# Kernel tuning notes

Hardware: AMD Instinct MI355X
Metric: run time of the kernel (lower is better)

## Reference

```python
import jax, jax.numpy as jnp
import numpy as np

ND, NA, E, EL, H, F = 100000, 50000, 500000, 200000, 128, 128


def setup_inputs() -> dict:
    key = jax.random.key(0)
    ks = jax.random.split(key, 20)
    def W(k, shape):
        return jax.random.normal(k, shape, dtype=jnp.float32) * 0.05
    inp = {
        'doc_x': jax.random.normal(ks[0], (ND, F), dtype=jnp.float32),
        'author_node_id': jnp.arange(NA, dtype=jnp.int64 if jax.config.jax_enable_x64 else jnp.int32),
        'edge_index': jnp.stack([
            jax.random.randint(ks[1], (E,), 0, ND),   # doc src
            jax.random.randint(ks[2], (E,), 0, NA),   # author dst
        ]),
        'edge_label_index': jnp.stack([
            jax.random.randint(ks[3], (EL,), 0, ND),
            jax.random.randint(ks[4], (EL,), 0, NA),
        ]),
        'doc_lin_W': W(ks[5], (F, H)), 'doc_lin_b': W(ks[6], (H,)),
        'author_emb': W(ks[7], (NA, H)),
        'c1_da_Wl': W(ks[8], (H, H)), 'c1_da_bl': W(ks[9], (H,)), 'c1_da_Wr': W(ks[10], (H, H)),
        'c1_ad_Wl': W(ks[11], (H, H)), 'c1_ad_bl': W(ks[12], (H,)), 'c1_ad_Wr': W(ks[13], (H, H)),
        'c2_da_Wl': W(ks[14], (H, H)), 'c2_da_bl': W(ks[15], (H,)), 'c2_da_Wr': W(ks[16], (H, H)),
        'c2_ad_Wl': W(ks[17], (H, H)), 'c2_ad_bl': W(ks[18], (H,)), 'c2_ad_Wr': W(ks[19], (H, H)),
    }
    return inp


def sage(x_src, x_dst, src, dst, num_dst, Wl, bl, Wr):
    # PyG SAGEConv (aggr='mean'): lin_l(mean_j x_src[j]) + lin_r(x_dst)
    msg = x_src[src]                                            # [E, H]
    agg = jax.ops.segment_sum(msg, dst, num_segments=num_dst)   # [num_dst, H]
    deg = jax.ops.segment_sum(jnp.ones_like(dst, dtype=x_src.dtype), dst, num_segments=num_dst)
    agg = agg / jnp.maximum(deg, 1.0)[:, None]
    return agg @ Wl + bl + x_dst @ Wr


def reference(doc_x, author_node_id, edge_index, edge_label_index,
              doc_lin_W, doc_lin_b, author_emb,
              c1_da_Wl, c1_da_bl, c1_da_Wr, c1_ad_Wl, c1_ad_bl, c1_ad_Wr,
              c2_da_Wl, c2_da_bl, c2_da_Wr, c2_ad_Wl, c2_ad_bl, c2_ad_Wr):
    x_doc = doc_x @ doc_lin_W + doc_lin_b          # [ND, H]
    x_author = author_emb[author_node_id]          # [NA, H]
    src_d, dst_a = edge_index[0], edge_index[1]
    # layer 1 (per-edge-type convs, to_hetero semantics) + ReLU
    h_a = sage(x_doc, x_author, src_d, dst_a, NA, c1_da_Wl, c1_da_bl, c1_da_Wr)
    h_d = sage(x_author, x_doc, dst_a, src_d, ND, c1_ad_Wl, c1_ad_bl, c1_ad_Wr)
    h_a, h_d = jax.nn.relu(h_a), jax.nn.relu(h_d)
    # layer 2
    o_a = sage(h_d, h_a, src_d, dst_a, NA, c2_da_Wl, c2_da_bl, c2_da_Wr)
    o_d = sage(h_a, h_d, dst_a, src_d, ND, c2_ad_Wl, c2_ad_bl, c2_ad_Wr)
    # edge scorer: dot product of gathered endpoint embeddings
    pred = (o_d[edge_label_index[0]] * o_a[edge_label_index[1]]).sum(-1)  # [EL]
    return pred
```

## Files before the change

### kernel.cpp

```cpp
#include <hip/hip_runtime.h>

typedef unsigned short u16;
typedef __attribute__((ext_vector_type(8))) short vbf16x8;
typedef __attribute__((ext_vector_type(4))) float vf32x4;

__device__ __forceinline__ float bf2f(u16 u) {
    union { unsigned int i; float f; } v; v.i = ((unsigned int)u) << 16; return v.f;
}
__device__ __forceinline__ u16 f2bf(float f) {
    union { float f; unsigned int i; } v; v.f = f;
    return (u16)((v.i + 0x7fffu + ((v.i >> 16) & 1u)) >> 16);
}

struct TPack { const float* src[9]; u16* dst[9]; };

#define NBUK 256
#define NBLK_BIN 256
#define SCAP 24
#define OVFCAP 32768
#define PACK_SH 17

__global__ __launch_bounds__(256) void mega_prep_bin(
    TPack p, const float* __restrict__ emb, const int* __restrict__ ids,
    u16* __restrict__ xauth, int NA,
    const int* __restrict__ src, const int* __restrict__ dst,
    unsigned* __restrict__ stageD, unsigned* __restrict__ stageA,
    int* __restrict__ cntD, int* __restrict__ cntA,
    uint2* __restrict__ ovfD, uint2* __restrict__ ovfA, int* __restrict__ ovfn,
    int E, int shD, int shA, int prepB) {
    int b = blockIdx.x;
    if (b >= prepB) {
        __shared__ int lcnt[NBUK];
        int bb = b - prepB;
        const bool isD = bb < NBLK_BIN;
        const int blk = isD ? bb : bb - NBLK_BIN;
        const int* key = isD ? src : dst;
        const int* val = isD ? dst : src;
        const int shift = isD ? shD : shA;
        unsigned* stage = isD ? stageD : stageA;
        int* cnt = isD ? cntD : cntA;
        uint2* ovf = isD ? ovfD : ovfA;
        int* on = ovfn + (isD ? 0 : 1);
        const int per = (E + NBLK_BIN - 1) / NBLK_BIN;
        const int beg = blk * per;
        const int end = min(beg + per, E);
        for (int i = threadIdx.x; i < NBUK; i += 256) lcnt[i] = 0;
        __syncthreads();
        for (int e = beg + (int)threadIdx.x; e < end; e += 256) {
            int k = key[e], v = val[e];
            int bkt = k >> shift;
            int slot = atomicAdd(&lcnt[bkt], 1);
            if (slot < SCAP) {
                unsigned local = (unsigned)(k - (bkt << shift));
                stage[((size_t)bkt * NBLK_BIN + blk) * SCAP + slot] =
                    (local << PACK_SH) | (unsigned)v;
            } else {
                int oi = atomicAdd(on, 1);
                if (oi < OVFCAP) ovf[oi] = make_uint2((unsigned)k, (unsigned)v);
            }
        }
        __syncthreads();
        for (int i = threadIdx.x; i < NBUK; i += 256)
            cnt[(size_t)i * NBLK_BIN + blk] = min(lcnt[i], SCAP);
        return;
    }
    if (b < 576) {
        int mat = b / 64;
        const float* s = p.src[mat];
        u16* d = p.dst[mat];
        int i = (b % 64) * 256 + threadIdx.x;
        int k = i >> 7, n = i & 127;
        d[(size_t)n * 128 + k] = f2bf(s[(size_t)k * 128 + n]);
    } else {
        int gid = (b - 576) * 256 + threadIdx.x;
        if (gid >= NA * 16) return;
        int n = gid >> 4, f = gid & 15;
        int id = ids[n];
        const float* s = emb + (size_t)id * 128 + f * 8;
        float4 lo = *(const float4*)(s);
        float4 hi = *(const float4*)(s + 4);
        u16 o[8] = {f2bf(lo.x), f2bf(lo.y), f2bf(lo.z), f2bf(lo.w),
                    f2bf(hi.x), f2bf(hi.y), f2bf(hi.z), f2bf(hi.w)};
        *(uint4*)(xauth + (size_t)n * 128 + f * 8) = *(const uint4*)o;
    }
}

__global__ __launch_bounds__(256) void bucket_count(
    const unsigned* __restrict__ stageD, const unsigned* __restrict__ stageA,
    const int* __restrict__ cntD, const int* __restrict__ cntA,
    const uint2* __restrict__ ovfD, const uint2* __restrict__ ovfA,
    const int* __restrict__ ovfn,
    int* __restrict__ cnt_d, int* __restrict__ cnt_a,
    int ND, int NA, int shD, int shA) {
    __shared__ int hist[1024];
    __shared__ int segc[NBLK_BIN];
    const bool isD = (int)blockIdx.x < NBUK;
    const int b = isD ? (int)blockIdx.x : (int)blockIdx.x - NBUK;
    const int sh = isD ? shD : shA;
    const int N = isD ? ND : NA;
    const int base = b << sh;
    const int range = min(1 << sh, N - base);
    if (range <= 0) return;
    const unsigned* stage = (isD ? stageD : stageA) + (size_t)b * NBLK_BIN * SCAP;
    const int* scnt = (isD ? cntD : cntA) + (size_t)b * NBLK_BIN;
    const uint2* ovf = isD ? ovfD : ovfA;
    const int nov = min(ovfn[isD ? 0 : 1], OVFCAP);
    int* out = isD ? cnt_d : cnt_a;
    const int tid = threadIdx.x;
    for (int i = tid; i < (1 << sh); i += 256) hist[i] = 0;
    segc[tid] = scnt[tid];
    __syncthreads();
    for (int j = tid; j < NBLK_BIN * SCAP; j += 256) {
        int seg = j / SCAP, slot = j - seg * SCAP;
        if (slot < segc[seg])
            atomicAdd(&hist[stage[j] >> PACK_SH], 1);
    }
    for (int i = tid; i < nov; i += 256) {
        int k = (int)ovf[i].x;
        if ((k >> sh) == b) atomicAdd(&hist[k - base], 1);
    }
    __syncthreads();
    for (int i = tid; i < range; i += 256) out[base + i] = hist[i];
}

__global__ __launch_bounds__(256) void scan1b(
    const int* __restrict__ cnt, int* __restrict__ incl,
    int* __restrict__ bs, int ND, int NA, int NBD) {
    __shared__ int sh[256];
    int b = blockIdx.x, tid = threadIdx.x;
    const int* in; int* out; int N; int lb;
    if (b < NBD) { in = cnt;      out = incl;      N = ND; lb = b; }
    else         { in = cnt + ND; out = incl + ND; N = NA; lb = b - NBD; }
    int gid = lb * 256 + tid;
    int v = gid < N ? in[gid] : 0;
    sh[tid] = v; __syncthreads();
    for (int off = 1; off < 256; off <<= 1) {
        int t = tid >= off ? sh[tid - off] : 0; __syncthreads();
        sh[tid] += t; __syncthreads();
    }
    if (gid < N) out[gid] = sh[tid];
    if (tid == 255) bs[b] = sh[255];
}

__global__ __launch_bounds__(256) void scan2b(int* __restrict__ bs, int NBD, int NBA) {
    __shared__ int sh[256];
    __shared__ int carry;
    int tid = threadIdx.x;
    for (int seg = 0; seg < 2; ++seg) {
        int* p = seg ? bs + NBD : bs;
        int nb = seg ? NBA : NBD;
        if (tid == 0) carry = 0;
        __syncthreads();
        for (int base = 0; base < nb; base += 256) {
            int i = base + tid;
            int v = i < nb ? p[i] : 0;
            sh[tid] = v; __syncthreads();
            for (int off = 1; off < 256; off <<= 1) {
                int t = tid >= off ? sh[tid - off] : 0; __syncthreads();
                sh[tid] += t; __syncthreads();
            }
            if (i < nb) p[i] = carry + sh[tid] - v;
            __syncthreads();
            if (tid == 255) carry += sh[255];
            __syncthreads();
        }
    }
}

__global__ __launch_bounds__(256) void scan3b(
    const int* __restrict__ incl, const int* __restrict__ bs,
    int* __restrict__ offs_d, int* __restrict__ offs_a,
    int ND, int NA, int NBD) {
    int b = blockIdx.x, tid = threadIdx.x;
    if (b < NBD) {
        int gid = b * 256 + tid;
        if (gid < ND) offs_d[gid + 1] = incl[gid] + bs[b];
        if (gid == 0) offs_d[0] = 0;
    } else {
        int gid = (b - NBD) * 256 + tid;
        if (gid < NA) offs_a[gid + 1] = incl[ND + gid] + bs[b];
        if (gid == 0) offs_a[0] = 0;
    }
}

__global__ __launch_bounds__(256) void bucket_fill2(
    const unsigned* __restrict__ stageD, const unsigned* __restrict__ stageA,
    const int* __restrict__ cntD, const int* __restrict__ cntA,
    const uint2* __restrict__ ovfD, const uint2* __restrict__ ovfA,
    const int* __restrict__ ovfn,
    const int* __restrict__ offs_d, const int* __restrict__ offs_a,
    int* __restrict__ nbr_d, int* __restrict__ nbr_a,
    int ND, int NA, int shD, int shA) {
    __shared__ int lcur[1024];
    __shared__ int segc[NBLK_BIN];
    const bool isD = (int)blockIdx.x < NBUK;
    const int b = isD ? (int)blockIdx.x : (int)blockIdx.x - NBUK;
    const int sh = isD ? shD : shA;
    const int N = isD ? ND : NA;
    const int base = b << sh;
    const int range = min(1 << sh, N - base);
    if (range <= 0) return;
    const unsigned* stage = (isD ? stageD : stageA) + (size_t)b * NBLK_BIN * SCAP;
    const int* scnt = (isD ? cntD : cntA) + (size_t)b * NBLK_BIN;
    const uint2* ovf = isD ? ovfD : ovfA;
    const int nov = min(ovfn[isD ? 0 : 1], OVFCAP);
    const int* offs = isD ? offs_d : offs_a;
    int* nbr = isD ? nbr_d : nbr_a;
    const int tid = threadIdx.x;
    for (int i = tid; i < range; i += 256) lcur[i] = offs[base + i];
    segc[tid] = scnt[tid];
    __syncthreads();
    for (int j = tid; j < NBLK_BIN * SCAP; j += 256) {
        int seg = j / SCAP, slot = j - seg * SCAP;
        if (slot < segc[seg]) {
            unsigned pk = stage[j];
            int local = pk >> PACK_SH;
            int v = (int)(pk & ((1u << PACK_SH) - 1u));
            nbr[atomicAdd(&lcur[local], 1)] = v;
        }
    }
    for (int i = tid; i < nov; i += 256) {
        int k = (int)ovf[i].x;
        if ((k >> sh) == b)
            nbr[atomicAdd(&lcur[k - base], 1)] = (int)ovf[i].y;
    }
}

__global__ __launch_bounds__(256) void agg_mean2(
    const u16* __restrict__ xa, const int* __restrict__ offs_a,
    const int* __restrict__ nbr_a, u16* __restrict__ outa, int NA,
    const u16* __restrict__ xd, const int* __restrict__ offs_d,
    const int* __restrict__ nbr_d, u16* __restrict__ outd, int ND) {
    int gid = blockIdx.x * 256 + threadIdx.x;
    int node = gid >> 4, f = gid & 15;
    int lane = threadIdx.x & 63;
    int gbase = lane & 48;
    const u16* x; const int* offs; const int* nbr; u16* out;
    if (node < NA) { x = xa; offs = offs_a; nbr = nbr_a; out = outa; }
    else {
        node -= NA;
        if (node >= ND) return;
        x = xd; offs = offs_d; nbr = nbr_d; out = outd;
    }
    int beg = offs[node], end = offs[node + 1];
    float acc[8] = {0, 0, 0, 0, 0, 0, 0, 0};

    for (int i = beg; i < end; i += 16) {
        int cnt = end - i; if (cnt > 16) cnt = 16;
        int myn = (i + f < end) ? nbr[i + f] : 0;
        int t = 0;
        for (; t + 3 < cnt; t += 4) {
            int i0 = __shfl(myn, gbase + t);
            int i1 = __shfl(myn, gbase + t + 1);
            int i2 = __shfl(myn, gbase + t + 2);
            int i3 = __shfl(myn, gbase + t + 3);
            uint4 q0 = *(const uint4*)(x + (size_t)i0 * 128 + f * 8);
            uint4 q1 = *(const uint4*)(x + (size_t)i1 * 128 + f * 8);
            uint4 q2 = *(const uint4*)(x + (size_t)i2 * 128 + f * 8);
            uint4 q3 = *(const uint4*)(x + (size_t)i3 * 128 + f * 8);
            acc[0] += bf2f((u16)(q0.x & 0xffff)) + bf2f((u16)(q1.x & 0xffff))
                    + bf2f((u16)(q2.x & 0xffff)) + bf2f((u16)(q3.x & 0xffff));
            acc[1] += bf2f((u16)(q0.x >> 16))    + bf2f((u16)(q1.x >> 16))
                    + bf2f((u16)(q2.x >> 16))    + bf2f((u16)(q3.x >> 16));
            acc[2] += bf2f((u16)(q0.y & 0xffff)) + bf2f((u16)(q1.y & 0xffff))
                    + bf2f((u16)(q2.y & 0xffff)) + bf2f((u16)(q3.y & 0xffff));
            acc[3] += bf2f((u16)(q0.y >> 16))    + bf2f((u16)(q1.y >> 16))
                    + bf2f((u16)(q2.y >> 16))    + bf2f((u16)(q3.y >> 16));
            acc[4] += bf2f((u16)(q0.z & 0xffff)) + bf2f((u16)(q1.z & 0xffff))
                    + bf2f((u16)(q2.z & 0xffff)) + bf2f((u16)(q3.z & 0xffff));
            acc[5] += bf2f((u16)(q0.z >> 16))    + bf2f((u16)(q1.z >> 16))
                    + bf2f((u16)(q2.z >> 16))    + bf2f((u16)(q3.z >> 16));
            acc[6] += bf2f((u16)(q0.w & 0xffff)) + bf2f((u16)(q1.w & 0xffff))
                    + bf2f((u16)(q2.w & 0xffff)) + bf2f((u16)(q3.w & 0xffff));
            acc[7] += bf2f((u16)(q0.w >> 16))    + bf2f((u16)(q1.w >> 16))
                    + bf2f((u16)(q2.w >> 16))    + bf2f((u16)(q3.w >> 16));
        }
        for (; t < cnt; ++t) {
            int i0 = __shfl(myn, gbase + t);
            uint4 q0 = *(const uint4*)(x + (size_t)i0 * 128 + f * 8);
            acc[0] += bf2f((u16)(q0.x & 0xffff));
            acc[1] += bf2f((u16)(q0.x >> 16));
            acc[2] += bf2f((u16)(q0.y & 0xffff));
            acc[3] += bf2f((u16)(q0.y >> 16));
            acc[4] += bf2f((u16)(q0.z & 0xffff));
            acc[5] += bf2f((u16)(q0.z >> 16));
            acc[6] += bf2f((u16)(q0.w & 0xffff));
            acc[7] += bf2f((u16)(q0.w >> 16));
        }
    }
    float inv = 1.0f / fmaxf((float)(end - beg), 1.0f);
    u16 o[8];
#pragma unroll
    for (int j = 0; j < 8; ++j) o[j] = f2bf(acc[j] * inv);
    *(uint4*)(out + (size_t)node * 128 + f * 8) = *(const uint4*)o;
}

__global__ __launch_bounds__(256) void doc_gemm4(
    const float* __restrict__ A1f, const u16* __restrict__ W1T,
    const float* __restrict__ bias, u16* __restrict__ out, const int M) {
    __shared__ u16 WS[128 * 128];
    const int tid = threadIdx.x;
    const int lane = tid & 63, wave = tid >> 6;
    const int r15 = lane & 15, kq = lane >> 4;
    const int rowbase = blockIdx.x * 128 + wave * 32;
    const int m0 = rowbase + r15, m1 = rowbase + 16 + r15;
    const bool v0 = rowbase < M, v1 = rowbase + 16 < M;

    const float4 z = {0.f, 0.f, 0.f, 0.f};
    float4 l0[4], h0[4], l1[4], h1[4];
#pragma unroll
    for (int ks = 0; ks < 4; ++ks) {
        const float* p0 = A1f + (size_t)m0 * 128 + ks * 32 + kq * 8;
        const float* p1 = A1f + (size_t)m1 * 128 + ks * 32 + kq * 8;
        l0[ks] = v0 ? *(const float4*)p0 : z;
        h0[ks] = v0 ? *(const float4*)(p0 + 4) : z;
        l1[ks] = v1 ? *(const float4*)p1 : z;
        h1[ks] = v1 ? *(const float4*)(p1 + 4) : z;
    }

#pragma unroll
    for (int i = 0; i < 8; ++i) {
        int L = i * 256 + tid;
        int n = L >> 4, bk = L & 15;
        *(uint4*)(WS + ((size_t)n * 16 + (bk ^ (n & 15))) * 8) =
            *(const uint4*)(W1T + (size_t)L * 8);
    }
    __syncthreads();

    vf32x4 acc0[8], acc1[8];
#pragma unroll
    for (int i = 0; i < 8; ++i) { acc0[i] = (vf32x4)(0.0f); acc1[i] = (vf32x4)(0.0f); }

#pragma unroll
    for (int ks = 0; ks < 4; ++ks) {
        vbf16x8 a0, a1;
        a0[0] = (short)f2bf(l0[ks].x); a0[1] = (short)f2bf(l0[ks].y);
        a0[2] = (short)f2bf(l0[ks].z); a0[3] = (short)f2bf(l0[ks].w);
        a0[4] = (short)f2bf(h0[ks].x); a0[5] = (short)f2bf(h0[ks].y);
        a0[6] = (short)f2bf(h0[ks].z); a0[7] = (short)f2bf(h0[ks].w);
        a1[0] = (short)f2bf(l1[ks].x); a1[1] = (short)f2bf(l1[ks].y);
        a1[2] = (short)f2bf(l1[ks].z); a1[3] = (short)f2bf(l1[ks].w);
        a1[4] = (short)f2bf(h1[ks].x); a1[5] = (short)f2bf(h1[ks].y);
        a1[6] = (short)f2bf(h1[ks].z); a1[7] = (short)f2bf(h1[ks].w);
#pragma unroll
        for (int nt = 0; nt < 8; ++nt) {
            vbf16x8 b = *(const vbf16x8*)(
                WS + ((size_t)(nt * 16 + r15) * 16 + ((ks * 4 + kq) ^ r15)) * 8);
            acc0[nt] = __builtin_amdgcn_mfma_f32_16x16x32_bf16(a0, b, acc0[nt], 0, 0, 0);
            acc1[nt] = __builtin_amdgcn_mfma_f32_16x16x32_bf16(a1, b, acc1[nt], 0, 0, 0);
        }
    }

#pragma unroll
    for (int nt = 0; nt < 8; ++nt) {
        const float bv = bias[nt * 16 + r15];
#pragma unroll
        for (int r = 0; r < 4; ++r) {
            if (v0) out[(size_t)(rowbase + kq * 4 + r) * 128 + nt * 16 + r15] =
                f2bf(acc0[nt][r] + bv);
            if (v1) out[(size_t)(rowbase + 16 + kq * 4 + r) * 128 + nt * 16 + r15] =
                f2bf(acc1[nt][r] + bv);
        }
    }
}

struct SideParams3 {
    const u16* A1b; const u16* W1T;
    const u16* A2b; const u16* W2T;
    const float* bias; u16* out;
    int M; int do_relu; int ntiles; int gblocks;
};
__global__ __launch_bounds__(256) void conv_gemm3(SideParams3 sa, SideParams3 sd) {
    __shared__ u16 WS[2 * 128 * 128];
    const bool isA = (int)blockIdx.x < sa.gblocks;
    SideParams3 P = isA ? sa : sd;
    const int gb = isA ? (int)blockIdx.x : (int)blockIdx.x - sa.gblocks;
    const int tid = threadIdx.x;
    const int lane = tid & 63, wave = tid >> 6;
    const int r15 = lane & 15, kq = lane >> 4;

#pragma unroll
    for (int i = 0; i < 8; ++i) {
        int L = i * 256 + tid;
        int n = L >> 4, bk = L & 15;
        *(uint4*)(WS + ((size_t)n * 16 + (bk ^ (n & 15))) * 8) =
            *(const uint4*)(P.W1T + (size_t)L * 8);
        *(uint4*)(WS + 16384 + ((size_t)n * 16 + (bk ^ (n & 15))) * 8) =
            *(const uint4*)(P.W2T + (size_t)L * 8);
    }
    __syncthreads();
    float bv[8];
#pragma unroll
    for (int nt = 0; nt < 8; ++nt) bv[nt] = P.bias[nt * 16 + r15];

    auto loadA = [&](const u16* Ab, int tile, vbf16x8* fa, vbf16x8* fb) {
        const int rowbase = tile * 128 + wave * 32;
        const int m0 = rowbase + r15, m1 = rowbase + 16 + r15;
        const bool v0 = rowbase < P.M, v1 = rowbase + 16 < P.M;
#pragma unroll
        for (int ks = 0; ks < 4; ++ks) {
            fa[ks] = v0 ? *(const vbf16x8*)(Ab + (size_t)m0 * 128 + ks * 32 + kq * 8)
                        : (vbf16x8)(short)0;
            fb[ks] = v1 ? *(const vbf16x8*)(Ab + (size_t)m1 * 128 + ks * 32 + kq * 8)
                        : (vbf16x8)(short)0;
        }
    };

    vbf16x8 c1a[4], c1b[4], c2a[4], c2b[4], n1a[4], n1b[4];
    if (gb < P.ntiles) loadA(P.A1b, gb, c1a, c1b);
    for (int t = gb; t < P.ntiles; t += P.gblocks) {
        loadA(P.A2b, t, c2a, c2b);
        const int tn = t + P.gblocks;
        if (tn < P.ntiles) loadA(P.A1b, tn, n1a, n1b);

        vf32x4 acc0[8], acc1[8];
#pragma unroll
        for (int i = 0; i < 8; ++i) { acc0[i] = (vf32x4)(0.0f); acc1[i] = (vf32x4)(0.0f); }
#pragma unroll
        for (int ks = 0; ks < 4; ++ks) {
#pragma unroll
            for (int nt = 0; nt < 8; ++nt) {
                vbf16x8 b = *(const vbf16x8*)(
                    WS + ((size_t)(nt * 16 + r15) * 16 + ((ks * 4 + kq) ^ r15)) * 8);
                acc0[nt] = __builtin_amdgcn_mfma_f32_16x16x32_bf16(c1a[ks], b, acc0[nt], 0, 0, 0);
                acc1[nt] = __builtin_amdgcn_mfma_f32_16x16x32_bf16(c1b[ks], b, acc1[nt], 0, 0, 0);
            }
        }
#pragma unroll
        for (int ks = 0; ks < 4; ++ks) {
#pragma unroll
            for (int nt = 0; nt < 8; ++nt) {
                vbf16x8 b = *(const vbf16x8*)(
                    WS + 16384 + ((size_t)(nt * 16 + r15) * 16 + ((ks * 4 + kq) ^ r15)) * 8);
                acc0[nt] = __builtin_amdgcn_mfma_f32_16x16x32_bf16(c2a[ks], b, acc0[nt], 0, 0, 0);
                acc1[nt] = __builtin_amdgcn_mfma_f32_16x16x32_bf16(c2b[ks], b, acc1[nt], 0, 0, 0);
            }
        }

        const int rowbase = t * 128 + wave * 32;
        const bool v0 = rowbase < P.M, v1 = rowbase + 16 < P.M;
#pragma unroll
        for (int nt = 0; nt < 8; ++nt) {
#pragma unroll
            for (int r = 0; r < 4; ++r) {
                if (v0) {
                    float v = acc0[nt][r] + bv[nt];
                    if (P.do_relu) v = fmaxf(v, 0.0f);
                    P.out[(size_t)(rowbase + kq * 4 + r) * 128 + nt * 16 + r15] = f2bf(v);
                }
                if (v1) {
                    float v = acc1[nt][r] + bv[nt];
                    if (P.do_relu) v = fmaxf(v, 0.0f);
                    P.out[(size_t)(rowbase + 16 + kq * 4 + r) * 128 + nt * 16 + r15] = f2bf(v);
                }
            }
        }
#pragma unroll
        for (int ks = 0; ks < 4; ++ks) { c1a[ks] = n1a[ks]; c1b[ks] = n1b[ks]; }
    }
}

__global__ __launch_bounds__(256) void edge_dot(
    const u16* __restrict__ od, const u16* __restrict__ oa,
    const int* __restrict__ i0, const int* __restrict__ i1,
    float* __restrict__ pred, int EL) {
    int gid = blockIdx.x * 256 + threadIdx.x;
    if (gid >= EL * 16) return;
    int e = gid >> 4, f = gid & 15;
    uint4 x = *(const uint4*)(od + (size_t)i0[e] * 128 + f * 8);
    uint4 y = *(const uint4*)(oa + (size_t)i1[e] * 128 + f * 8);
    float s = 0.0f;
    s += bf2f((u16)(x.x & 0xffff)) * bf2f((u16)(y.x & 0xffff));
    s += bf2f((u16)(x.x >> 16))    * bf2f((u16)(y.x >> 16));
    s += bf2f((u16)(x.y & 0xffff)) * bf2f((u16)(y.y & 0xffff));
    s += bf2f((u16)(x.y >> 16))    * bf2f((u16)(y.y >> 16));
    s += bf2f((u16)(x.z & 0xffff)) * bf2f((u16)(y.z & 0xffff));
    s += bf2f((u16)(x.z >> 16))    * bf2f((u16)(y.z >> 16));
    s += bf2f((u16)(x.w & 0xffff)) * bf2f((u16)(y.w & 0xffff));
    s += bf2f((u16)(x.w >> 16))    * bf2f((u16)(y.w >> 16));
    s += __shfl_xor(s, 1);
    s += __shfl_xor(s, 2);
    s += __shfl_xor(s, 4);
    s += __shfl_xor(s, 8);
    if (f == 0) pred[e] = s;
}

extern "C" void kernel_launch(void* const* d_in, const int* in_sizes, int n_in,
                              void* d_out, int out_size, void* d_ws, size_t ws_size,
                              hipStream_t stream) {
    const float* doc_x    = (const float*)d_in[0];
    const int*   auth_id  = (const int*)d_in[1];
    const int*   eidx     = (const int*)d_in[2];
    const int*   elidx    = (const int*)d_in[3];
    const float* W_doc    = (const float*)d_in[4];
    const float* b_doc    = (const float*)d_in[5];
    const float* emb      = (const float*)d_in[6];
    const float* c1_da_Wl = (const float*)d_in[7];
    const float* c1_da_bl = (const float*)d_in[8];
    const float* c1_da_Wr = (const float*)d_in[9];
    const float* c1_ad_Wl = (const float*)d_in[10];
    const float* c1_ad_bl = (const float*)d_in[11];
    const float* c1_ad_Wr = (const float*)d_in[12];
    const float* c2_da_Wl = (const float*)d_in[13];
    const float* c2_da_bl = (const float*)d_in[14];
    const float* c2_da_Wr = (const float*)d_in[15];
    const float* c2_ad_Wl = (const float*)d_in[16];
    const float* c2_ad_bl = (const float*)d_in[17];
    const float* c2_ad_Wr = (const float*)d_in[18];

    const int ND = in_sizes[0] / 128;
    const int NA = in_sizes[1];
    const int E  = in_sizes[2] / 2;
    const int EL = in_sizes[3] / 2;
    const int* e_src = eidx;
    const int* e_dst = eidx + E;
    const int NBD = (ND + 255) / 256, NBA = (NA + 255) / 256;
    const int BA = (NA + 127) / 128, BD = (ND + 127) / 128;
    const int prepB = 576 + (NA * 16 + 255) / 256;

    char* base = (char*)d_ws;
    size_t off = 0;
    auto alloc = [&](size_t bytes) {
        void* p = base + off;
        off = (off + bytes + 255) & ~(size_t)255;
        return p;
    };
    u16*  xdoc  = (u16*)alloc((size_t)ND * 128 * 2);
    u16*  xauth = (u16*)alloc((size_t)NA * 128 * 2);
    u16*  hd    = (u16*)alloc((size_t)ND * 128 * 2);
    u16*  ha    = (u16*)alloc((size_t)NA * 128 * 2);
    u16*  aggA  = (u16*)alloc((size_t)NA * 128 * 2);
    u16*  aggD  = (u16*)alloc((size_t)ND * 128 * 2);
    u16*  wt    = (u16*)alloc((size_t)9 * 128 * 128 * 2);
    int*  cnt   = (int*)alloc((size_t)(ND + NA) * 4);
    int*  incl  = (int*)alloc((size_t)(ND + NA) * 4);
    int*  bs    = (int*)alloc((size_t)(NBD + NBA) * 4);
    int*  offs_d = (int*)alloc((size_t)(ND + 1) * 4);
    int*  offs_a = (int*)alloc((size_t)(NA + 1) * 4);
    int*  nbr_d = (int*)alloc((size_t)E * 4);
    int*  nbr_a = (int*)alloc((size_t)E * 4);
    int*  cntD  = (int*)alloc((size_t)NBUK * NBLK_BIN * 4);
    int*  cntA  = (int*)alloc((size_t)NBUK * NBLK_BIN * 4);
    uint2* ovfD = (uint2*)alloc((size_t)OVFCAP * 8);
    uint2* ovfA = (uint2*)alloc((size_t)OVFCAP * 8);
    int*  ovfn  = (int*)alloc(256);
    (void)ws_size; (void)n_in; (void)out_size;
    u16* od = xdoc;
    u16* oa = xauth;
    unsigned* stageD = (unsigned*)aggD;
    unsigned* stageA = (unsigned*)aggA;

    TPack tp;
    const float* srcs[9] = {W_doc, c1_da_Wl, c1_da_Wr, c1_ad_Wl, c1_ad_Wr,
                            c2_da_Wl, c2_da_Wr, c2_ad_Wl, c2_ad_Wr};
    for (int i = 0; i < 9; ++i) { tp.src[i] = srcs[i]; tp.dst[i] = wt + (size_t)i * 16384; }
    const u16 *WTdoc = wt, *WT_c1daL = wt + 16384, *WT_c1daR = wt + 2 * 16384,
              *WT_c1adL = wt + 3 * 16384, *WT_c1adR = wt + 4 * 16384,
              *WT_c2daL = wt + 5 * 16384, *WT_c2daR = wt + 6 * 16384,
              *WT_c2adL = wt + 7 * 16384, *WT_c2adR = wt + 8 * 16384;

    int shD = 0; while (((ND - 1) >> shD) >= NBUK) ++shD;
    int shA = 0; while (((NA - 1) >> shA) >= NBUK) ++shA;

    hipMemsetAsync(ovfn, 0, 8, stream);
    mega_prep_bin<<<prepB + 2 * NBLK_BIN, 256, 0, stream>>>(
        tp, emb, auth_id, xauth, NA, e_src, e_dst,
        stageD, stageA, cntD, cntA, ovfD, ovfA, ovfn, E, shD, shA, prepB);

    bucket_count<<<2 * NBUK, 256, 0, stream>>>(
        stageD, stageA, cntD, cntA, ovfD, ovfA, ovfn, cnt, cnt + ND,
        ND, NA, shD, shA);

    scan1b<<<NBD + NBA, 256, 0, stream>>>(cnt, incl, bs, ND, NA, NBD);
    scan2b<<<1, 256, 0, stream>>>(bs, NBD, NBA);
    scan3b<<<NBD + NBA, 256, 0, stream>>>(incl, bs, offs_d, offs_a, ND, NA, NBD);

    bucket_fill2<<<2 * NBUK, 256, 0, stream>>>(
        stageD, stageA, cntD, cntA, ovfD, ovfA, ovfn, offs_d, offs_a,
        nbr_d, nbr_a, ND, NA, shD, shA);

    doc_gemm4<<<BD, 256, 0, stream>>>(doc_x, WTdoc, b_doc, xdoc, ND);

    const int aggGrid = ((NA + ND) * 16 + 255) / 256;
    const int gA = (int)(((long)512 * BA) / (BA + BD));
    const int gD = 512 - gA;

    agg_mean2<<<aggGrid, 256, 0, stream>>>(
        xdoc, offs_a, nbr_a, aggA, NA, xauth, offs_d, nbr_d, aggD, ND);
    {
        SideParams3 sa = {aggA, WT_c1daL, xauth, WT_c1daR, c1_da_bl, ha, NA, 1, BA, gA};
        SideParams3 sd = {aggD, WT_c1adL, xdoc,  WT_c1adR, c1_ad_bl, hd, ND, 1, BD, gD};
        conv_gemm3<<<gA + gD, 256, 0, stream>>>(sa, sd);
    }

    agg_mean2<<<aggGrid, 256, 0, stream>>>(
        hd, offs_a, nbr_a, aggA, NA, ha, offs_d, nbr_d, aggD, ND);
    {
        SideParams3 sa = {aggA, WT_c2daL, ha, WT_c2daR, c2_da_bl, oa, NA, 0, BA, gA};
        SideParams3 sd = {aggD, WT_c2adL, hd, WT_c2adR, c2_ad_bl, od, ND, 0, BD, gD};
        conv_gemm3<<<gA + gD, 256, 0, stream>>>(sa, sd);
    }

    edge_dot<<<(EL * 16 + 255) / 256, 256, 0, stream>>>(
        od, oa, elidx, elidx + EL, (float*)d_out, EL);
}
```

Measured before the change: 381.2 us.

## Fuse doc GEMM into binning kernel and replace three-pass scan with bucket-level scan

The weight transpose moves into its own small kernel, which also zeroes the overflow counters in place of the memset. The doc linear GEMM is folded into the same launch as the edge binning and author gather, so these independent jobs run concurrently. The three-kernel global prefix scan is replaced by per-bucket totals from the count kernel, one small scan over 512 values, and a local scan inside the fill kernel. This cuts kernel launches and global round trips. In exchange, the mega kernel now always reserves 32KB of shared memory for every block type, and the doc GEMM no longer prefetches A before loading weights.

```diff
diff --git a/kernel.cpp b/kernel.cpp
--- a/kernel.cpp
+++ b/kernel.cpp
@@ -20,18 +20,96 @@
 #define OVFCAP 32768
 #define PACK_SH 17
 
-__global__ __launch_bounds__(256) void mega_prep_bin(
-    TPack p, const float* __restrict__ emb, const int* __restrict__ ids,
+__global__ __launch_bounds__(256) void wtp(TPack p, int* __restrict__ ovfn) {
+    int b = blockIdx.x;
+    if (b == 0 && threadIdx.x < 2) ovfn[threadIdx.x] = 0;
+    int mat = b >> 6;
+    const float* s = p.src[mat];
+    u16* d = p.dst[mat];
+    int i = (b & 63) * 256 + threadIdx.x;
+    int k = i >> 7, n = i & 127;
+    d[(size_t)n * 128 + k] = f2bf(s[(size_t)k * 128 + n]);
+}
+
+__global__ __launch_bounds__(256) void mega2(
+    const float* __restrict__ A1f, const u16* __restrict__ W1T,
+    const float* __restrict__ biasd, u16* __restrict__ xdoc, int M, int BD,
+    const float* __restrict__ emb, const int* __restrict__ ids,
     u16* __restrict__ xauth, int NA,
     const int* __restrict__ src, const int* __restrict__ dst,
     unsigned* __restrict__ stageD, unsigned* __restrict__ stageA,
     int* __restrict__ cntD, int* __restrict__ cntA,
     uint2* __restrict__ ovfD, uint2* __restrict__ ovfA, int* __restrict__ ovfn,
-    int E, int shD, int shA, int prepB) {
-    int b = blockIdx.x;
-    if (b >= prepB) {
-        __shared__ int lcnt[NBUK];
-        int bb = b - prepB;
+    int E, int shD, int shA) {
+    __shared__ u16 WS[128 * 128];
+    const int b = blockIdx.x;
+    const int tid = threadIdx.x;
+
+    if (b < BD) {
+        const int lane = tid & 63, wave = tid >> 6;
+        const int r15 = lane & 15, kq = lane >> 4;
+        const int rowbase = b * 128 + wave * 32;
+        const int m0 = rowbase + r15, m1 = rowbase + 16 + r15;
+        const bool v0 = rowbase < M, v1 = rowbase + 16 < M;
+
+        vf32x4 acc0[8], acc1[8];
+#pragma unroll
+        for (int i = 0; i < 8; ++i) { acc0[i] = (vf32x4)(0.0f); acc1[i] = (vf32x4)(0.0f); }
+
+#pragma unroll
+        for (int i = 0; i < 8; ++i) {
+            int L = i * 256 + tid;
+            int n = L >> 4, bk = L & 15;
+            *(uint4*)(WS + ((size_t)n * 16 + (bk ^ (n & 15))) * 8) =
+                *(const uint4*)(W1T + (size_t)L * 8);
+        }
+        __syncthreads();
+
+#pragma unroll
+        for (int ks = 0; ks < 4; ++ks) {
+            vbf16x8 a0 = (vbf16x8)(short)0, a1 = (vbf16x8)(short)0;
+            if (v0) {
+                const float* p = A1f + (size_t)m0 * 128 + ks * 32 + kq * 8;
+                float4 lo = *(const float4*)p, hi = *(const float4*)(p + 4);
+                a0[0] = (short)f2bf(lo.x); a0[1] = (short)f2bf(lo.y);
+                a0[2] = (short)f2bf(lo.z); a0[3] = (short)f2bf(lo.w);
+                a0[4] = (short)f2bf(hi.x); a0[5] = (short)f2bf(hi.y);
+                a0[6] = (short)f2bf(hi.z); a0[7] = (short)f2bf(hi.w);
+            }
+            if (v1) {
+                const float* p = A1f + (size_t)m1 * 128 + ks * 32 + kq * 8;
+                float4 lo = *(const float4*)p, hi = *(const float4*)(p + 4);
+                a1[0] = (short)f2bf(lo.x); a1[1] = (short)f2bf(lo.y);
+                a1[2] = (short)f2bf(lo.z); a1[3] = (short)f2bf(lo.w);
+                a1[4] = (short)f2bf(hi.x); a1[5] = (short)f2bf(hi.y);
+                a1[6] = (short)f2bf(hi.z); a1[7] = (short)f2bf(hi.w);
+            }
+#pragma unroll
+            for (int nt = 0; nt < 8; ++nt) {
+                vbf16x8 bb = *(const vbf16x8*)(
+                    WS + ((size_t)(nt * 16 + r15) * 16 + ((ks * 4 + kq) ^ r15)) * 8);
+                acc0[nt] = __builtin_amdgcn_mfma_f32_16x16x32_bf16(a0, bb, acc0[nt], 0, 0, 0);
+                acc1[nt] = __builtin_amdgcn_mfma_f32_16x16x32_bf16(a1, bb, acc1[nt], 0, 0, 0);
+            }
+        }
+
+#pragma unroll
+        for (int nt = 0; nt < 8; ++nt) {
+            const float bv = biasd[nt * 16 + r15];
+#pragma unroll
+            for (int r = 0; r < 4; ++r) {
+                if (v0) xdoc[(size_t)(rowbase + kq * 4 + r) * 128 + nt * 16 + r15] =
+                    f2bf(acc0[nt][r] + bv);
+                if (v1) xdoc[(size_t)(rowbase + 16 + kq * 4 + r) * 128 + nt * 16 + r15] =
+                    f2bf(acc1[nt][r] + bv);
+            }
+        }
+        return;
+    }
+
+    if (b < BD + 2 * NBLK_BIN) {
+        int* lcnt = (int*)WS;
+        int bb = b - BD;
         const bool isD = bb < NBLK_BIN;
         const int blk = isD ? bb : bb - NBLK_BIN;
         const int* key = isD ? src : dst;
@@ -44,9 +122,9 @@
         const int per = (E + NBLK_BIN - 1) / NBLK_BIN;
         const int beg = blk * per;
         const int end = min(beg + per, E);
-        for (int i = threadIdx.x; i < NBUK; i += 256) lcnt[i] = 0;
-        __syncthreads();
-        for (int e = beg + (int)threadIdx.x; e < end; e += 256) {
+        for (int i = tid; i < NBUK; i += 256) lcnt[i] = 0;
+        __syncthreads();
+        for (int e = beg + tid; e < end; e += 256) {
             int k = key[e], v = val[e];
             int bkt = k >> shift;
             int slot = atomicAdd(&lcnt[bkt], 1);
@@ -60,155 +138,140 @@
             }
         }
         __syncthreads();
-        for (int i = threadIdx.x; i < NBUK; i += 256)
+        for (int i = tid; i < NBUK; i += 256)
             cnt[(size_t)i * NBLK_BIN + blk] = min(lcnt[i], SCAP);
         return;
     }
-    if (b < 576) {
-        int mat = b / 64;
-        const float* s = p.src[mat];
-        u16* d = p.dst[mat];
-        int i = (b % 64) * 256 + threadIdx.x;
-        int k = i >> 7, n = i & 127;
-        d[(size_t)n * 128 + k] = f2bf(s[(size_t)k * 128 + n]);
-    } else {
-        int gid = (b - 576) * 256 + threadIdx.x;
-        if (gid >= NA * 16) return;
-        int n = gid >> 4, f = gid & 15;
-        int id = ids[n];
-        const float* s = emb + (size_t)id * 128 + f * 8;
-        float4 lo = *(const float4*)(s);
-        float4 hi = *(const float4*)(s + 4);
-        u16 o[8] = {f2bf(lo.x), f2bf(lo.y), f2bf(lo.z), f2bf(lo.w),
-                    f2bf(hi.x), f2bf(hi.y), f2bf(hi.z), f2bf(hi.w)};
-        *(uint4*)(xauth + (size_t)n * 128 + f * 8) = *(const uint4*)o;
-    }
-}
-
-__global__ __launch_bounds__(256) void bucket_count(
+
+    int gid = (b - BD - 2 * NBLK_BIN) * 256 + tid;
+    if (gid >= NA * 16) return;
+    int n = gid >> 4, f = gid & 15;
+    int id = ids[n];
+    const float* s = emb + (size_t)id * 128 + f * 8;
+    float4 lo = *(const float4*)(s);
+    float4 hi = *(const float4*)(s + 4);
+    u16 o[8] = {f2bf(lo.x), f2bf(lo.y), f2bf(lo.z), f2bf(lo.w),
+                f2bf(hi.x), f2bf(hi.y), f2bf(hi.z), f2bf(hi.w)};
+    *(uint4*)(xauth + (size_t)n * 128 + f * 8) = *(const uint4*)o;
+}
+
+__global__ __launch_bounds__(256) void bucket_count2(
     const unsigned* __restrict__ stageD, const unsigned* __restrict__ stageA,
     const int* __restrict__ cntD, const int* __restrict__ cntA,
     const uint2* __restrict__ ovfD, const uint2* __restrict__ ovfA,
     const int* __restrict__ ovfn,
-    int* __restrict__ cnt_d, int* __restrict__ cnt_a,
+    int* __restrict__ cnt_d, int* __restrict__ cnt_a, int* __restrict__ btot,
     int ND, int NA, int shD, int shA) {
     __shared__ int hist[1024];
     __shared__ int segc[NBLK_BIN];
+    __shared__ int red[256];
     const bool isD = (int)blockIdx.x < NBUK;
     const int b = isD ? (int)blockIdx.x : (int)blockIdx.x - NBUK;
     const int sh = isD ? shD : shA;
     const int N = isD ? ND : NA;
     const int base = b << sh;
     const int range = min(1 << sh, N - base);
+    const int tid = threadIdx.x;
+    if (range <= 0) { if (tid == 0) btot[blockIdx.x] = 0; return; }
+    const unsigned* stage = (isD ? stageD : stageA) + (size_t)b * NBLK_BIN * SCAP;
+    const int* scnt = (isD ? cntD : cntA) + (size_t)b * NBLK_BIN;
+    const uint2* ovf = isD ? ovfD : ovfA;
+    const int nov = min(ovfn[isD ? 0 : 1], OVFCAP);
+    int* out = isD ? cnt_d : cnt_a;
+    for (int i = tid; i < (1 << sh); i += 256) hist[i] = 0;
+    segc[tid] = scnt[tid];
+    __syncthreads();
+    int my = 0;
+    for (int j = tid; j < NBLK_BIN * SCAP; j += 256) {
+        int seg = j / SCAP, slot = j - seg * SCAP;
+        if (slot < segc[seg]) { atomicAdd(&hist[stage[j] >> PACK_SH], 1); ++my; }
+    }
+    for (int i = tid; i < nov; i += 256) {
+        int k = (int)ovf[i].x;
+        if ((k >> sh) == b) { atomicAdd(&hist[k - base], 1); ++my; }
+    }
+    red[tid] = my;
+    __syncthreads();
+    for (int s = 128; s > 0; s >>= 1) {
+        if (tid < s) red[tid] += red[tid + s];
+        __syncthreads();
+    }
+    if (tid == 0) btot[blockIdx.x] = red[0];
+    for (int i = tid; i < range; i += 256) out[base + i] = hist[i];
+}
+
+__global__ __launch_bounds__(256) void scanb(int* __restrict__ btot) {
+    __shared__ int sh[256];
+    const int tid = threadIdx.x;
+    for (int seg = 0; seg < 2; ++seg) {
+        int* p = btot + seg * NBUK;
+        int v = p[tid];
+        sh[tid] = v;
+        __syncthreads();
+        for (int off = 1; off < 256; off <<= 1) {
+            int t = tid >= off ? sh[tid - off] : 0;
+            __syncthreads();
+            sh[tid] += t;
+            __syncthreads();
+        }
+        p[tid] = sh[tid] - v;
+        __syncthreads();
+    }
+}
+
+__global__ __launch_bounds__(256) void bucket_fill3(
+    const unsigned* __restrict__ stageD, const unsigned* __restrict__ stageA,
+    const int* __restrict__ cntD, const int* __restrict__ cntA,
+    const uint2* __restrict__ ovfD, const uint2* __restrict__ ovfA,
+    const int* __restrict__ ovfn,
+    const int* __restrict__ cnt_d, const int* __restrict__ cnt_a,
+    const int* __restrict__ btot,
+    int* __restrict__ offs_d, int* __restrict__ offs_a,
+    int* __restrict__ nbr_d, int* __restrict__ nbr_a,
+    int ND, int NA, int shD, int shA) {
+    __shared__ int lcur[1024];
+    __shared__ int segc[NBLK_BIN];
+    __shared__ int sh[256];
+    __shared__ int carry;
+    const bool isD = (int)blockIdx.x < NBUK;
+    const int b = isD ? (int)blockIdx.x : (int)blockIdx.x - NBUK;
+    const int shft = isD ? shD : shA;
+    const int N = isD ? ND : NA;
+    const int base = b << shft;
+    const int range = min(1 << shft, N - base);
     if (range <= 0) return;
     const unsigned* stage = (isD ? stageD : stageA) + (size_t)b * NBLK_BIN * SCAP;
     const int* scnt = (isD ? cntD : cntA) + (size_t)b * NBLK_BIN;
     const uint2* ovf = isD ? ovfD : ovfA;
     const int nov = min(ovfn[isD ? 0 : 1], OVFCAP);
-    int* out = isD ? cnt_d : cnt_a;
-    const int tid = threadIdx.x;
-    for (int i = tid; i < (1 << sh); i += 256) hist[i] = 0;
-    segc[tid] = scnt[tid];
-    __syncthreads();
-    for (int j = tid; j < NBLK_BIN * SCAP; j += 256) {
-        int seg = j / SCAP, slot = j - seg * SCAP;
-        if (slot < segc[seg])
-            atomicAdd(&hist[stage[j] >> PACK_SH], 1);
-    }
-    for (int i = tid; i < nov; i += 256) {
-        int k = (int)ovf[i].x;
-        if ((k >> sh) == b) atomicAdd(&hist[k - base], 1);
-    }
-    __syncthreads();
-    for (int i = tid; i < range; i += 256) out[base + i] = hist[i];
-}
-
-__global__ __launch_bounds__(256) void scan1b(
-    const int* __restrict__ cnt, int* __restrict__ incl,
-    int* __restrict__ bs, int ND, int NA, int NBD) {
-    __shared__ int sh[256];
-    int b = blockIdx.x, tid = threadIdx.x;
-    const int* in; int* out; int N; int lb;
-    if (b < NBD) { in = cnt;      out = incl;      N = ND; lb = b; }
-    else         { in = cnt + ND; out = incl + ND; N = NA; lb = b - NBD; }
-    int gid = lb * 256 + tid;
-    int v = gid < N ? in[gid] : 0;
-    sh[tid] = v; __syncthreads();
-    for (int off = 1; off < 256; off <<= 1) {
-        int t = tid >= off ? sh[tid - off] : 0; __syncthreads();
-        sh[tid] += t; __syncthreads();
-    }
-    if (gid < N) out[gid] = sh[tid];
-    if (tid == 255) bs[b] = sh[255];
-}
-
-__global__ __launch_bounds__(256) void scan2b(int* __restrict__ bs, int NBD, int NBA) {
-    __shared__ int sh[256];
-    __shared__ int carry;
-    int tid = threadIdx.x;
-    for (int seg = 0; seg < 2; ++seg) {
-        int* p = seg ? bs + NBD : bs;
-        int nb = seg ? NBA : NBD;
-        if (tid == 0) carry = 0;
-        __syncthreads();
-        for (int base = 0; base < nb; base += 256) {
-            int i = base + tid;
-            int v = i < nb ? p[i] : 0;
-            sh[tid] = v; __syncthreads();
-            for (int off = 1; off < 256; off <<= 1) {
-                int t = tid >= off ? sh[tid - off] : 0; __syncthreads();
-                sh[tid] += t; __syncthreads();
-            }
-            if (i < nb) p[i] = carry + sh[tid] - v;
-            __syncthreads();
-            if (tid == 255) carry += sh[255];
-            __syncthreads();
-        }
-    }
-}
-
-__global__ __launch_bounds__(256) void scan3b(
-    const int* __restrict__ incl, const int* __restrict__ bs,
-    int* __restrict__ offs_d, int* __restrict__ offs_a,
-    int ND, int NA, int NBD) {
-    int b = blockIdx.x, tid = threadIdx.x;
-    if (b < NBD) {
-        int gid = b * 256 + tid;
-        if (gid < ND) offs_d[gid + 1] = incl[gid] + bs[b];
-        if (gid == 0) offs_d[0] = 0;
-    } else {
-        int gid = (b - NBD) * 256 + tid;
-        if (gid < NA) offs_a[gid + 1] = incl[ND + gid] + bs[b];
-        if (gid == 0) offs_a[0] = 0;
-    }
-}
-
-__global__ __launch_bounds__(256) void bucket_fill2(
-    const unsigned* __restrict__ stageD, const unsigned* __restrict__ stageA,
-    const int* __restrict__ cntD, const int* __restrict__ cntA,
-    const uint2* __restrict__ ovfD, const uint2* __restrict__ ovfA,
-    const int* __restrict__ ovfn,
-    const int* __restrict__ offs_d, const int* __restrict__ offs_a,
-    int* __restrict__ nbr_d, int* __restrict__ nbr_a,
-    int ND, int NA, int shD, int shA) {
-    __shared__ int lcur[1024];
-    __shared__ int segc[NBLK_BIN];
-    const bool isD = (int)blockIdx.x < NBUK;
-    const int b = isD ? (int)blockIdx.x : (int)blockIdx.x - NBUK;
-    const int sh = isD ? shD : shA;
-    const int N = isD ? ND : NA;
-    const int base = b << sh;
-    const int range = min(1 << sh, N - base);
-    if (range <= 0) return;
-    const unsigned* stage = (isD ? stageD : stageA) + (size_t)b * NBLK_BIN * SCAP;
-    const int* scnt = (isD ? cntD : cntA) + (size_t)b * NBLK_BIN;
-    const uint2* ovf = isD ? ovfD : ovfA;
-    const int nov = min(ovfn[isD ? 0 : 1], OVFCAP);
-    const int* offs = isD ? offs_d : offs_a;
+    const int* cnodes = isD ? cnt_d : cnt_a;
+    int* offs = isD ? offs_d : offs_a;
     int* nbr = isD ? nbr_d : nbr_a;
     const int tid = threadIdx.x;
-    for (int i = tid; i < range; i += 256) lcur[i] = offs[base + i];
     segc[tid] = scnt[tid];
+    if (tid == 0) carry = btot[blockIdx.x];
+    __syncthreads();
+    for (int c0 = 0; c0 < range; c0 += 256) {
+        int i = c0 + tid;
+        int v = (i < range) ? cnodes[base + i] : 0;
+        sh[tid] = v;
+        __syncthreads();
+        for (int off = 1; off < 256; off <<= 1) {
+            int t = tid >= off ? sh[tid - off] : 0;
+            __syncthreads();
+            sh[tid] += t;
+            __syncthreads();
+        }
+        if (i < range) {
+            int ex = carry + sh[tid] - v;
+            lcur[i] = ex;
+            offs[base + i] = ex;
+        }
+        __syncthreads();
+        if (tid == 255) carry += sh[255];
+        __syncthreads();
+    }
+    if (tid == 0) offs[base + range] = carry;
     __syncthreads();
     for (int j = tid; j < NBLK_BIN * SCAP; j += 256) {
         int seg = j / SCAP, slot = j - seg * SCAP;
@@ -221,7 +284,7 @@
     }
     for (int i = tid; i < nov; i += 256) {
         int k = (int)ovf[i].x;
-        if ((k >> sh) == b)
+        if ((k >> shft) == b)
             nbr[atomicAdd(&lcur[k - base], 1)] = (int)ovf[i].y;
     }
 }
@@ -295,75 +358,6 @@
     *(uint4*)(out + (size_t)node * 128 + f * 8) = *(const uint4*)o;
 }
 
-__global__ __launch_bounds__(256) void doc_gemm4(
-    const float* __restrict__ A1f, const u16* __restrict__ W1T,
-    const float* __restrict__ bias, u16* __restrict__ out, const int M) {
-    __shared__ u16 WS[128 * 128];
-    const int tid = threadIdx.x;
-    const int lane = tid & 63, wave = tid >> 6;
-    const int r15 = lane & 15, kq = lane >> 4;
-    const int rowbase = blockIdx.x * 128 + wave * 32;
-    const int m0 = rowbase + r15, m1 = rowbase + 16 + r15;
-    const bool v0 = rowbase < M, v1 = rowbase + 16 < M;
-
-    const float4 z = {0.f, 0.f, 0.f, 0.f};
-    float4 l0[4], h0[4], l1[4], h1[4];
-#pragma unroll
-    for (int ks = 0; ks < 4; ++ks) {
-        const float* p0 = A1f + (size_t)m0 * 128 + ks * 32 + kq * 8;
-        const float* p1 = A1f + (size_t)m1 * 128 + ks * 32 + kq * 8;
-        l0[ks] = v0 ? *(const float4*)p0 : z;
-        h0[ks] = v0 ? *(const float4*)(p0 + 4) : z;
-        l1[ks] = v1 ? *(const float4*)p1 : z;
-        h1[ks] = v1 ? *(const float4*)(p1 + 4) : z;
-    }
-
-#pragma unroll
-    for (int i = 0; i < 8; ++i) {
-        int L = i * 256 + tid;
-        int n = L >> 4, bk = L & 15;
-        *(uint4*)(WS + ((size_t)n * 16 + (bk ^ (n & 15))) * 8) =
-            *(const uint4*)(W1T + (size_t)L * 8);
-    }
-    __syncthreads();
-
-    vf32x4 acc0[8], acc1[8];
-#pragma unroll
-    for (int i = 0; i < 8; ++i) { acc0[i] = (vf32x4)(0.0f); acc1[i] = (vf32x4)(0.0f); }
-
-#pragma unroll
-    for (int ks = 0; ks < 4; ++ks) {
-        vbf16x8 a0, a1;
-        a0[0] = (short)f2bf(l0[ks].x); a0[1] = (short)f2bf(l0[ks].y);
-        a0[2] = (short)f2bf(l0[ks].z); a0[3] = (short)f2bf(l0[ks].w);
-        a0[4] = (short)f2bf(h0[ks].x); a0[5] = (short)f2bf(h0[ks].y);
-        a0[6] = (short)f2bf(h0[ks].z); a0[7] = (short)f2bf(h0[ks].w);
-        a1[0] = (short)f2bf(l1[ks].x); a1[1] = (short)f2bf(l1[ks].y);
-        a1[2] = (short)f2bf(l1[ks].z); a1[3] = (short)f2bf(l1[ks].w);
-        a1[4] = (short)f2bf(h1[ks].x); a1[5] = (short)f2bf(h1[ks].y);
-        a1[6] = (short)f2bf(h1[ks].z); a1[7] = (short)f2bf(h1[ks].w);
-#pragma unroll
-        for (int nt = 0; nt < 8; ++nt) {
-            vbf16x8 b = *(const vbf16x8*)(
-                WS + ((size_t)(nt * 16 + r15) * 16 + ((ks * 4 + kq) ^ r15)) * 8);
-            acc0[nt] = __builtin_amdgcn_mfma_f32_16x16x32_bf16(a0, b, acc0[nt], 0, 0, 0);
-            acc1[nt] = __builtin_amdgcn_mfma_f32_16x16x32_bf16(a1, b, acc1[nt], 0, 0, 0);
-        }
-    }
-
-#pragma unroll
-    for (int nt = 0; nt < 8; ++nt) {
-        const float bv = bias[nt * 16 + r15];
-#pragma unroll
-        for (int r = 0; r < 4; ++r) {
-            if (v0) out[(size_t)(rowbase + kq * 4 + r) * 128 + nt * 16 + r15] =
-                f2bf(acc0[nt][r] + bv);
-            if (v1) out[(size_t)(rowbase + 16 + kq * 4 + r) * 128 + nt * 16 + r15] =
-                f2bf(acc1[nt][r] + bv);
-        }
-    }
-}
-
 struct SideParams3 {
     const u16* A1b; const u16* W1T;
     const u16* A2b; const u16* W2T;
@@ -514,9 +508,8 @@
     const int EL = in_sizes[3] / 2;
     const int* e_src = eidx;
     const int* e_dst = eidx + E;
-    const int NBD = (ND + 255) / 256, NBA = (NA + 255) / 256;
     const int BA = (NA + 127) / 128, BD = (ND + 127) / 128;
-    const int prepB = 576 + (NA * 16 + 255) / 256;
+    const int gatherB = (NA * 16 + 255) / 256;
 
     char* base = (char*)d_ws;
     size_t off = 0;
@@ -533,14 +526,13 @@
     u16*  aggD  = (u16*)alloc((size_t)ND * 128 * 2);
     u16*  wt    = (u16*)alloc((size_t)9 * 128 * 128 * 2);
     int*  cnt   = (int*)alloc((size_t)(ND + NA) * 4);
-    int*  incl  = (int*)alloc((size_t)(ND + NA) * 4);
-    int*  bs    = (int*)alloc((size_t)(NBD + NBA) * 4);
     int*  offs_d = (int*)alloc((size_t)(ND + 1) * 4);
     int*  offs_a = (int*)alloc((size_t)(NA + 1) * 4);
     int*  nbr_d = (int*)alloc((size_t)E * 4);
     int*  nbr_a = (int*)alloc((size_t)E * 4);
     int*  cntD  = (int*)alloc((size_t)NBUK * NBLK_BIN * 4);
     int*  cntA  = (int*)alloc((size_t)NBUK * NBLK_BIN * 4);
+    int*  btot  = (int*)alloc((size_t)2 * NBUK * 4);
     uint2* ovfD = (uint2*)alloc((size_t)OVFCAP * 8);
     uint2* ovfA = (uint2*)alloc((size_t)OVFCAP * 8);
     int*  ovfn  = (int*)alloc(256);
@@ -562,24 +554,24 @@
     int shD = 0; while (((ND - 1) >> shD) >= NBUK) ++shD;
     int shA = 0; while (((NA - 1) >> shA) >= NBUK) ++shA;
 
-    hipMemsetAsync(ovfn, 0, 8, stream);
-    mega_prep_bin<<<prepB + 2 * NBLK_BIN, 256, 0, stream>>>(
-        tp, emb, auth_id, xauth, NA, e_src, e_dst,
-        stageD, stageA, cntD, cntA, ovfD, ovfA, ovfn, E, shD, shA, prepB);
-
-    bucket_count<<<2 * NBUK, 256, 0, stream>>>(
-        stageD, stageA, cntD, cntA, ovfD, ovfA, ovfn, cnt, cnt + ND,
+    wtp<<<576, 256, 0, stream>>>(tp, ovfn);
+
+    mega2<<<BD + 2 * NBLK_BIN + gatherB, 256, 0, stream>>>(
+        doc_x, WTdoc, b_doc, xdoc, ND, BD,
+        emb, auth_id, xauth, NA,
+        e_src, e_dst, stageD, stageA, cntD, cntA, ovfD, ovfA, ovfn,
+        E, shD, shA);
+
+    bucket_count2<<<2 * NBUK, 256, 0, stream>>>(
+        stageD, stageA, cntD, cntA, ovfD, ovfA, ovfn,
+        cnt, cnt + ND, btot, ND, NA, shD, shA);
+
+    scanb<<<1, 256, 0, stream>>>(btot);
+
+    bucket_fill3<<<2 * NBUK, 256, 0, stream>>>(
+        stageD, stageA, cntD, cntA, ovfD, ovfA, ovfn,
+        cnt, cnt + ND, btot, offs_d, offs_a, nbr_d, nbr_a,
         ND, NA, shD, shA);
-
-    scan1b<<<NBD + NBA, 256, 0, stream>>>(cnt, incl, bs, ND, NA, NBD);
-    scan2b<<<1, 256, 0, stream>>>(bs, NBD, NBA);
-    scan3b<<<NBD + NBA, 256, 0, stream>>>(incl, bs, offs_d, offs_a, ND, NA, NBD);
-
-    bucket_fill2<<<2 * NBUK, 256, 0, stream>>>(
-        stageD, stageA, cntD, cntA, ovfD, ovfA, ovfn, offs_d, offs_a,
-        nbr_d, nbr_a, ND, NA, shD, shA);
-
-    doc_gemm4<<<BD, 256, 0, stream>>>(doc_x, WTdoc, b_doc, xdoc, ND);
 
     const int aggGrid = ((NA + ND) * 16 + 255) / 256;
     const int gA = (int)(((long)512 * BA) / (BA + BD));
```

After: 354.8 us (median of 2 runs). 1.07x faster.
